# Kernel tuning notes

Hardware: AMD Instinct MI355X
Metric: run time of the kernel (lower is better)

The kernel has to match this reference:

```python
import jax, jax.numpy as jnp
import numpy as np
from jax import lax

B, T, D, NL, NH, FF, NC, SMAX, MAXS = 4, 160000, 768, 12, 12, 2048, 100, 64, 200
CONV_SPEC = [(512, 10, 5), (512, 3, 2), (512, 3, 2), (512, 3, 2), (512, 2, 2), (512, 2, 2), (768, 2, 2)]
TP = 499  # frames after conv stack for T=160000


def _ln(x, w, b, eps=1e-5):
    m = x.mean(-1, keepdims=True)
    v = ((x - m) ** 2).mean(-1, keepdims=True)
    return (x - m) * lax.rsqrt(v + eps) * w + b


def setup_inputs() -> dict:
    key = jax.random.key(0)
    ks = iter(jax.random.split(key, 64))
    d = {}
    d['x'] = jax.random.normal(next(ks), (B, 1, T), jnp.float32)
    d['seg_bounds'] = jnp.sort(jax.random.randint(next(ks), (B, SMAX + 1), 0, TP), axis=-1)
    d['n_segs'] = jax.random.randint(next(ks), (B,), SMAX // 2, SMAX + 1)
    in_c = 1
    for i, (oc, k, s) in enumerate(CONV_SPEC):
        d[f'conv_w{i}'] = jax.random.normal(next(ks), (oc, in_c, k), jnp.float32) * 0.02
        d[f'conv_b{i}'] = jnp.zeros((oc,), jnp.float32)
        in_c = oc
    d['attn_v'] = jax.random.normal(next(ks), (D,), jnp.float32)  # torch.randn init
    d['pos_emb'] = jax.random.normal(next(ks), (MAXS, D), jnp.float32) * 0.02
    d['in_w'] = jax.random.normal(next(ks), (NL, 3 * D, D), jnp.float32) * 0.02
    d['in_b'] = jnp.zeros((NL, 3 * D), jnp.float32)
    d['out_w'] = jax.random.normal(next(ks), (NL, D, D), jnp.float32) * 0.02
    d['out_b'] = jnp.zeros((NL, D), jnp.float32)
    d['ff1_w'] = jax.random.normal(next(ks), (NL, FF, D), jnp.float32) * 0.02
    d['ff1_b'] = jnp.zeros((NL, FF), jnp.float32)
    d['ff2_w'] = jax.random.normal(next(ks), (NL, D, FF), jnp.float32) * 0.02
    d['ff2_b'] = jnp.zeros((NL, D), jnp.float32)
    d['ln1_w'] = jnp.ones((NL, D), jnp.float32)
    d['ln1_b'] = jnp.zeros((NL, D), jnp.float32)
    d['ln2_w'] = jnp.ones((NL, D), jnp.float32)
    d['ln2_b'] = jnp.zeros((NL, D), jnp.float32)
    d['fln_w'] = jnp.ones((D,), jnp.float32)
    d['fln_b'] = jnp.zeros((D,), jnp.float32)
    d['proj_w'] = jax.random.normal(next(ks), (NC, D), jnp.float32) * 0.02
    d['proj_b'] = jnp.zeros((NC,), jnp.float32)
    return d


def reference(x, seg_bounds, n_segs,
              conv_w0, conv_b0, conv_w1, conv_b1, conv_w2, conv_b2, conv_w3, conv_b3,
              conv_w4, conv_b4, conv_w5, conv_b5, conv_w6, conv_b6,
              attn_v, pos_emb, in_w, in_b, out_w, out_b,
              ff1_w, ff1_b, ff2_w, ff2_b, ln1_w, ln1_b, ln2_w, ln2_b,
              fln_w, fln_b, proj_w, proj_b):
    # ---- conv feature extractor (Conv1d + ReLU stack), NCW layout ----
    ws = [conv_w0, conv_w1, conv_w2, conv_w3, conv_w4, conv_w5, conv_w6]
    bs = [conv_b0, conv_b1, conv_b2, conv_b3, conv_b4, conv_b5, conv_b6]
    h = x
    for w, b, (_, _, s) in zip(ws, bs, CONV_SPEC):
        h = lax.conv_general_dilated(h, w, (s,), 'VALID',
                                     dimension_numbers=('NCH', 'OIH', 'NCH'))
        h = jax.nn.relu(h + b[None, :, None])
    feats = h.transpose(0, 2, 1)  # [B, Tp, D]
    Tp = feats.shape[1]

    # ---- vectorized per-segment attention pooling (replaces ragged python loop) ----
    starts = jnp.clip(seg_bounds[:, :-1], 0, Tp - 1)           # [B, Smax]
    ends = jnp.maximum(starts + 1, jnp.clip(seg_bounds[:, 1:], 0, Tp))
    pad_mask = jnp.arange(SMAX)[None, :] >= n_segs[:, None]    # [B, Smax] True=pad
    t = jnp.arange(Tp)
    fm = (t[None, None, :] >= starts[..., None]) & (t[None, None, :] < ends[..., None]) \
         & (~pad_mask[..., None])                              # [B, Smax, Tp]
    scores = jnp.einsum('btc,c->bt', feats, attn_v)[:, None, :]  # [B, 1, Tp]
    m = jnp.max(jnp.where(fm, scores, -jnp.inf), axis=-1, keepdims=True)
    m = jnp.where(jnp.isfinite(m), m, 0.0)
    e = jnp.where(fm, jnp.exp(scores - m), 0.0)
    den = e.sum(-1, keepdims=True)
    wgt = e / jnp.where(den > 0, den, 1.0)                     # masked softmax over frames
    tokens = jnp.einsum('bst,btc->bsc', wgt, feats)            # [B, Smax, D]; pads are zeros

    tokens = tokens + pos_emb[:SMAX][None]

    # ---- post-norm transformer encoder (torch TransformerEncoderLayer defaults) ----
    dh = D // NH
    scale = 1.0 / np.sqrt(dh)

    def layer(tok, p):
        iw, ib, ow, ob, f1w, f1b, f2w, f2b, l1w, l1b, l2w, l2b = p
        qkv = tok @ iw.T + ib
        q, k, v = jnp.split(qkv, 3, axis=-1)
        def heads(z):
            return z.reshape(B, SMAX, NH, dh).transpose(0, 2, 1, 3)
        q, k, v = heads(q), heads(k), heads(v)
        att = jnp.einsum('bhqd,bhkd->bhqk', q, k) * scale
        att = jnp.where(pad_mask[:, None, None, :], -1e9, att)  # key padding mask
        att = jax.nn.softmax(att, axis=-1)
        o = jnp.einsum('bhqk,bhkd->bhqd', att, v).transpose(0, 2, 1, 3).reshape(B, SMAX, D)
        o = o @ ow.T + ob
        tok = _ln(tok + o, l1w, l1b)
        f = jax.nn.relu(tok @ f1w.T + f1b) @ f2w.T + f2b
        tok = _ln(tok + f, l2w, l2b)
        return tok, None

    tokens, _ = lax.scan(layer, tokens,
                         (in_w, in_b, out_w, out_b, ff1_w, ff1_b, ff2_w, ff2_b,
                          ln1_w, ln1_b, ln2_w, ln2_b))

    y = _ln(tokens, fln_w, fln_b)
    logits = y @ proj_w.T + proj_b
    return logits, pad_mask
```

## Files before the change

### kernel.cpp

```cpp
#include <hip/hip_runtime.h>
#include <hip/hip_bf16.h>

#define BATCH 4
#define TIN0 160000
#define DMODEL 768
#define NLAYER 12
#define FFDIM 2048
#define NCLS 100
#define SMAX_ 64
#define TP_ 499

typedef __attribute__((ext_vector_type(8))) short short8;
typedef __attribute__((ext_vector_type(4))) float f32x4;

__device__ inline ushort f2b(float f) { __hip_bfloat16 h = __float2bfloat16(f); return *(ushort*)&h; }
__device__ inline float b2f(ushort u) { __hip_bfloat16 h = *(__hip_bfloat16*)&u; return __bfloat162float(h); }

__device__ inline void gl_lds16(const ushort* g, ushort* l) {
    __builtin_amdgcn_global_load_lds((const __attribute__((address_space(1))) unsigned int*)g,
                                     (__attribute__((address_space(3))) unsigned int*)l, 16, 0, 0);
}

__device__ inline float wave_reduce_sum(float v) {
#pragma unroll
    for (int off = 32; off > 0; off >>= 1) v += __shfl_down(v, off, 64);
    return v;
}
__device__ inline float wave_reduce_max(float v) {
#pragma unroll
    for (int off = 32; off > 0; off >>= 1) v = fmaxf(v, __shfl_down(v, off, 64));
    return v;
}
__device__ inline float block_reduce_sum(float v, float* scratch) {
    v = wave_reduce_sum(v);
    int wid = threadIdx.x >> 6;
    if ((threadIdx.x & 63) == 0) scratch[wid] = v;
    __syncthreads();
    float r = scratch[0] + scratch[1] + scratch[2] + scratch[3];
    __syncthreads();
    return r;
}
__device__ inline float block_reduce_max(float v, float* scratch) {
    v = wave_reduce_max(v);
    int wid = threadIdx.x >> 6;
    if ((threadIdx.x & 63) == 0) scratch[wid] = v;
    __syncthreads();
    float r = fmaxf(fmaxf(scratch[0], scratch[1]), fmaxf(scratch[2], scratch[3]));
    __syncthreads();
    return r;
}

template <int KW>
__global__ __launch_bounds__(256) void convT_mfma(
    const ushort* __restrict__ A,
    const ushort* __restrict__ Wc,
    const float* __restrict__ bias,
    ushort* __restrict__ outp,
    int Cin, int Cout, int Tout,
    int tBase, int uBase, int uMax,
    long aStride, long oStride) {
    constexpr int EB = 132;
    __shared__ ushort sA[288 * 64];
    __shared__ ushort sB[KW * 128 * 32];
    const int tid = threadIdx.x;
    const int lane = tid & 63;
    const int wv = tid >> 6;
    const int mrow = lane & 15;
    const int kq = lane >> 4;
    const int t0 = tBase + blockIdx.x * 128;
    const int oc0 = blockIdx.y * 128;
    const ushort* Ab = A + (size_t)blockIdx.z * aStride;
    ushort* outb = outp + (size_t)blockIdx.z * oStride;
    const int K = KW * Cin;

    f32x4 acc[2][8];
#pragma unroll
    for (int s = 0; s < 2; s++)
#pragma unroll
        for (int n = 0; n < 8; n++) acc[s][n] = (f32x4){0.f, 0.f, 0.f, 0.f};

    const int nC8 = Cin >> 6;
    for (int c8 = 0; c8 < nC8; c8++) {
        const int ic0 = c8 << 6;
#pragma unroll
        for (int rd = 0; rd < 9; rd++) {
            int slotBase = rd * 256 + wv * 64;
            int slot = slotBase + lane;
            int r = slot >> 3;
            int g = (slot & 7) ^ (r & 7);
            int u = (r < EB) ? (2 * t0 + 2 * r) : (2 * t0 + 2 * (r - EB) + 1);
            u -= uBase;
            if (u < 0) u = 0;
            if (u > uMax) u = uMax;
            gl_lds16(Ab + (size_t)u * Cin + ic0 + g * 8, &sA[slotBase * 8]);
        }
#pragma unroll
        for (int h = 0; h < 2; h++) {
#pragma unroll
            for (int rd = 0; rd < KW * 2; rd++) {
                int slotBase = rd * 256 + wv * 64;
                int slot = slotBase + lane;
                int r = slot >> 2;
                int g = (slot & 3) ^ ((r >> 1) & 3);
                int ocr = oc0 + (r & 127);
                if (ocr > Cout - 1) ocr = Cout - 1;
                int kwi = r >> 7;
                gl_lds16(Wc + (size_t)ocr * K + kwi * Cin + ic0 + h * 32 + g * 8,
                         &sB[slotBase * 8]);
            }
            __syncthreads();
#pragma unroll
            for (int kw = 0; kw < KW; kw++) {
                const int abase = (kw & 1) ? EB : 0;
                const int aoff = kw >> 1;
#pragma unroll
                for (int s = 0; s < 2; s++) {
                    int ar = abase + wv * 32 + s * 16 + mrow + aoff;
                    short8 af = *(const short8*)&sA[ar * 64 + (((h * 4 + kq) ^ (ar & 7)) * 8)];
#pragma unroll
                    for (int n = 0; n < 8; n++) {
                        int br = kw * 128 + n * 16 + mrow;
                        short8 bf = *(const short8*)&sB[br * 32 + ((kq ^ ((br >> 1) & 3)) * 8)];
                        acc[s][n] = __builtin_amdgcn_mfma_f32_16x16x32_bf16(af, bf, acc[s][n], 0, 0, 0);
                    }
                }
            }
            __syncthreads();
        }
    }

    float bz[8];
#pragma unroll
    for (int n = 0; n < 8; n++) {
        int oc = oc0 + n * 16 + mrow;
        bz[n] = (oc < Cout) ? bias[oc] : 0.f;
    }
#pragma unroll
    for (int s = 0; s < 2; s++) {
        int tb = t0 + wv * 32 + s * 16 + kq * 4;
#pragma unroll
        for (int n = 0; n < 8; n++) {
            int oc = oc0 + n * 16 + mrow;
            if (oc >= Cout) continue;
#pragma unroll
            for (int r = 0; r < 4; r++) {
                int t = tb + r;
                if (t < Tout) outb[(size_t)t * Cout + oc] = f2b(fmaxf(acc[s][n][r] + bz[n], 0.f));
            }
        }
    }
}

template <int KW, int STRIDE, int RELU, int OBF, int BF32>
__global__ __launch_bounds__(256) void conv_mfma(
    const ushort* __restrict__ A,
    const ushort* __restrict__ Wc,
    const float* __restrict__ Wf,
    const float* __restrict__ bias,
    void* __restrict__ outv,
    int Cin, int Cout, int Tout, int tBase, int uBase,
    long aStride, long oStride) {
    const int K = KW * Cin;
    const int nCh = K >> 5;
    const int t0 = tBase + blockIdx.x * 128;
    const int oc0 = blockIdx.y * 128;
    const int b = blockIdx.z;
    const ushort* Ab = A + (size_t)b * aStride;
    __shared__ ushort sA[4096];
    __shared__ ushort sB[4096];
    const int tid = threadIdx.x;
    const int lane = tid & 63;
    const int wv = tid >> 6;
    const int rsub = lane >> 2;
    const int kgW = (lane & 3) ^ ((lane >> 3) & 3);
    const int mrow = lane & 15;
    const int kq = lane >> 4;
    const int slot8 = (mrow * 4 + (kq ^ ((mrow >> 1) & 3))) * 8;

    f32x4 acc[2][8];
#pragma unroll
    for (int s = 0; s < 2; s++)
#pragma unroll
        for (int n = 0; n < 8; n++) acc[s][n] = (f32x4){0.f, 0.f, 0.f, 0.f};

    for (int c = 0; c < nCh; c++) {
#pragma unroll
        for (int j = 0; j < 2; j++) {
            int t = t0 + j * 64 + wv * 16 + rsub;
            if (t > Tout - 1) t = Tout - 1;
            int u = STRIDE * t - uBase;
            gl_lds16(Ab + (size_t)u * Cin + c * 32 + kgW * 8, &sA[(j * 64 + wv * 16) * 32]);
        }
#pragma unroll
        for (int j = 0; j < 2; j++) {
            int rowb = oc0 + j * 64 + wv * 16 + rsub;
            if (rowb > Cout - 1) rowb = Cout - 1;
            if (BF32) {
                const float* wp = Wf + (size_t)rowb * K + c * 32 + kgW * 8;
                float4 w0_ = *(const float4*)wp;
                float4 w1_ = *(const float4*)(wp + 4);
                short8 vals;
                vals[0] = (short)f2b(w0_.x); vals[1] = (short)f2b(w0_.y);
                vals[2] = (short)f2b(w0_.z); vals[3] = (short)f2b(w0_.w);
                vals[4] = (short)f2b(w1_.x); vals[5] = (short)f2b(w1_.y);
                vals[6] = (short)f2b(w1_.z); vals[7] = (short)f2b(w1_.w);
                *(short8*)&sB[(j * 64 + wv * 16) * 32 + lane * 8] = vals;
            } else {
                gl_lds16(Wc + (size_t)rowb * K + c * 32 + kgW * 8, &sB[(j * 64 + wv * 16) * 32]);
            }
        }
        __syncthreads();
        short8 a0 = *(const short8*)&sA[(wv * 32 + 0) * 32 + slot8];
        short8 a1 = *(const short8*)&sA[(wv * 32 + 16) * 32 + slot8];
#pragma unroll
        for (int n = 0; n < 8; n++) {
            short8 bf = *(const short8*)&sB[(n * 16) * 32 + slot8];
            acc[0][n] = __builtin_amdgcn_mfma_f32_16x16x32_bf16(a0, bf, acc[0][n], 0, 0, 0);
            acc[1][n] = __builtin_amdgcn_mfma_f32_16x16x32_bf16(a1, bf, acc[1][n], 0, 0, 0);
        }
        __syncthreads();
    }
    float* outf = (float*)outv + (size_t)b * oStride;
    ushort* outh = (ushort*)outv + (size_t)b * oStride;
    float bz[8];
#pragma unroll
    for (int n = 0; n < 8; n++) {
        int oc = oc0 + n * 16 + mrow;
        bz[n] = (oc < Cout) ? bias[oc] : 0.f;
    }
#pragma unroll
    for (int s = 0; s < 2; s++) {
        int tb = t0 + wv * 32 + s * 16 + kq * 4;
#pragma unroll
        for (int n = 0; n < 8; n++) {
            int oc = oc0 + n * 16 + mrow;
            if (oc >= Cout) continue;
#pragma unroll
            for (int r = 0; r < 4; r++) {
                int t = tb + r;
                if (t < Tout) {
                    float v = acc[s][n][r] + bz[n];
                    if (RELU) v = fmaxf(v, 0.f);
                    if (OBF) outh[(size_t)t * Cout + oc] = f2b(v);
                    else outf[(size_t)t * Cout + oc] = v;
                }
            }
        }
    }
}

__global__ __launch_bounds__(256) void gemm_sk(
    const ushort* __restrict__ A, const float* __restrict__ Wf,
    const float* __restrict__ bias, float* __restrict__ outp,
    int M, int K, int KCH, long oSlab) {
    __shared__ ushort sA[4096];
    __shared__ ushort sB[4096];
    const int tid = threadIdx.x;
    const int lane = tid & 63;
    const int wv = tid >> 6;
    const int rsub = lane >> 2;
    const int kgW = (lane & 3) ^ ((lane >> 3) & 3);
    const int mrow = lane & 15;
    const int kq = lane >> 4;
    const int slot8 = (mrow * 4 + (kq ^ ((mrow >> 1) & 3))) * 8;
    const int t0 = blockIdx.x * 128;
    const int oc0 = blockIdx.y * 128;
    const int kc = blockIdx.z;
    const int k0 = kc * KCH;

    f32x4 acc[2][8];
#pragma unroll
    for (int s = 0; s < 2; s++)
#pragma unroll
        for (int n = 0; n < 8; n++) acc[s][n] = (f32x4){0.f, 0.f, 0.f, 0.f};

    const int nIt = KCH >> 5;
    for (int c = 0; c < nIt; c++) {
        const int kk = k0 + (c << 5);
#pragma unroll
        for (int j = 0; j < 2; j++) {
            int t = t0 + j * 64 + wv * 16 + rsub;
            gl_lds16(A + (size_t)t * K + kk + kgW * 8, &sA[(j * 64 + wv * 16) * 32]);
        }
#pragma unroll
        for (int j = 0; j < 2; j++) {
            int rowb = oc0 + j * 64 + wv * 16 + rsub;
            const float* wp = Wf + (size_t)rowb * K + kk + kgW * 8;
            float4 w0_ = *(const float4*)wp;
            float4 w1_ = *(const float4*)(wp + 4);
            short8 vals;
            vals[0] = (short)f2b(w0_.x); vals[1] = (short)f2b(w0_.y);
            vals[2] = (short)f2b(w0_.z); vals[3] = (short)f2b(w0_.w);
            vals[4] = (short)f2b(w1_.x); vals[5] = (short)f2b(w1_.y);
            vals[6] = (short)f2b(w1_.z); vals[7] = (short)f2b(w1_.w);
            *(short8*)&sB[(j * 64 + wv * 16) * 32 + lane * 8] = vals;
        }
        __syncthreads();
        short8 a0 = *(const short8*)&sA[(wv * 32 + 0) * 32 + slot8];
        short8 a1 = *(const short8*)&sA[(wv * 32 + 16) * 32 + slot8];
#pragma unroll
        for (int n = 0; n < 8; n++) {
            short8 bf = *(const short8*)&sB[(n * 16) * 32 + slot8];
            acc[0][n] = __builtin_amdgcn_mfma_f32_16x16x32_bf16(a0, bf, acc[0][n], 0, 0, 0);
            acc[1][n] = __builtin_amdgcn_mfma_f32_16x16x32_bf16(a1, bf, acc[1][n], 0, 0, 0);
        }
        __syncthreads();
    }

    float* op = outp + (size_t)kc * oSlab;
#pragma unroll
    for (int s = 0; s < 2; s++) {
        int tb = t0 + wv * 32 + s * 16 + kq * 4;
#pragma unroll
        for (int n = 0; n < 8; n++) {
            int oc = oc0 + n * 16 + mrow;
            float bz = (kc == 0) ? bias[oc] : 0.f;
#pragma unroll
            for (int r = 0; r < 4; r++) {
                op[(size_t)(tb + r) * M + oc] = acc[s][n][r] + bz;
            }
        }
    }
}

__global__ __launch_bounds__(256) void relu_cast(const float* __restrict__ p,
                                                 ushort* __restrict__ o,
                                                 long n, long slab, int nP) {
    for (long i = (long)blockIdx.x * 1024 + threadIdx.x; i < n; i += (long)gridDim.x * 1024) {
#pragma unroll
        for (int j = 0; j < 4; j++) {
            long k = i + (long)j * 256;
            if (k < n) {
                float v = 0.f;
                for (int q = 0; q < nP; q++) v += p[k + q * slab];
                o[k] = f2b(fmaxf(v, 0.f));
            }
        }
    }
}

__global__ __launch_bounds__(256) void conv0_mfma(const float* __restrict__ x,
                                                  const ushort* __restrict__ w0pad,
                                                  const float* __restrict__ b0,
                                                  ushort* __restrict__ c0,
                                                  int uBase, int nU) {
    __shared__ ushort sA[4096];
    __shared__ ushort sB[4096];
    const int tid = threadIdx.x;
    const int lane = tid & 63;
    const int wv = tid >> 6;
    const int rsub = lane >> 2;
    const int kgW = (lane & 3) ^ ((lane >> 3) & 3);
    const int mrow = lane & 15;
    const int kq = lane >> 4;
    const int slot8 = (mrow * 4 + (kq ^ ((mrow >> 1) & 3))) * 8;
    const int r0 = blockIdx.x * 128;
    const int oc0 = blockIdx.y * 128;

    f32x4 acc[2][8];
#pragma unroll
    for (int s = 0; s < 2; s++)
#pragma unroll
        for (int n = 0; n < 8; n++) acc[s][n] = (f32x4){0.f, 0.f, 0.f, 0.f};

#pragma unroll
    for (int j = 0; j < 2; j++) {
        int r = r0 + j * 64 + wv * 16 + rsub;
        if (r > nU - 1) r = nU - 1;
        const float* xp = x + (size_t)5 * (uBase + r);
        short8 vals = (short8){0, 0, 0, 0, 0, 0, 0, 0};
        if (kgW == 0) {
#pragma unroll
            for (int q = 0; q < 8; q++) vals[q] = (short)f2b(xp[q]);
        } else if (kgW == 1) {
            vals[0] = (short)f2b(xp[8]);
            vals[1] = (short)f2b(xp[9]);
        }
        *(short8*)&sA[(j * 64 + wv * 16) * 32 + lane * 8] = vals;
    }
#pragma unroll
    for (int j = 0; j < 2; j++) {
        int rowb = oc0 + j * 64 + wv * 16 + rsub;
        gl_lds16(w0pad + (size_t)rowb * 32 + kgW * 8, &sB[(j * 64 + wv * 16) * 32]);
    }
    __syncthreads();
    short8 a0 = *(const short8*)&sA[(wv * 32 + 0) * 32 + slot8];
    short8 a1 = *(const short8*)&sA[(wv * 32 + 16) * 32 + slot8];
#pragma unroll
    for (int n = 0; n < 8; n++) {
        short8 bf = *(const short8*)&sB[(n * 16) * 32 + slot8];
        acc[0][n] = __builtin_amdgcn_mfma_f32_16x16x32_bf16(a0, bf, acc[0][n], 0, 0, 0);
        acc[1][n] = __builtin_amdgcn_mfma_f32_16x16x32_bf16(a1, bf, acc[1][n], 0, 0, 0);
    }
#pragma unroll
    for (int s = 0; s < 2; s++) {
        int rb = r0 + wv * 32 + s * 16 + kq * 4;
#pragma unroll
        for (int n = 0; n < 8; n++) {
            int oc = oc0 + n * 16 + mrow;
            float bz = b0[oc];
#pragma unroll
            for (int r = 0; r < 4; r++) {
                int rr = rb + r;
                if (rr < nU) c0[(size_t)rr * 512 + oc] = f2b(fmaxf(acc[s][n][r] + bz, 0.f));
            }
        }
    }
}

__global__ __launch_bounds__(256) void convw_kernel(
    const float* __restrict__ w1, const float* __restrict__ w2, const float* __restrict__ w3,
    const float* __restrict__ w4, const float* __restrict__ w5, const float* __restrict__ w6,
    const float* __restrict__ w0, ushort* __restrict__ dst, ushort* __restrict__ dw0) {
    const int z = blockIdx.y;
    const int COUTS[6] = {512, 512, 512, 512, 512, 768};
    const int KWS[6] = {3, 3, 3, 2, 2, 2};
    const long OFFS[6] = {0, 786432, 1572864, 2359296, 2883584, 3407872};
    const float* srcs[6] = {w1, w2, w3, w4, w5, w6};
    if (z == 6) {
        for (int o = blockIdx.x * 256 + threadIdx.x; o < 512 * 32; o += gridDim.x * 256) {
            int oc = o >> 5, q = o & 31;
            dw0[o] = (q < 10) ? f2b(w0[oc * 10 + q]) : (ushort)0;
        }
        return;
    }
    const float* src = srcs[z];
    ushort* d = dst + OFFS[z];
    const int Cin = 512, Kw = KWS[z];
    const int K = Cin * Kw;
    const long n = (long)COUTS[z] * K;
    for (long o = blockIdx.x * 256 + threadIdx.x; o < n; o += (long)gridDim.x * 256) {
        long oc = o / K;
        int rem = (int)(o - oc * K);
        int kw = rem / Cin, ic = rem - kw * Cin;
        d[o] = f2b(src[(oc * Cin + ic) * Kw + kw]);
    }
}

__global__ __launch_bounds__(256) void scores_kernel(const ushort* __restrict__ feats,
                                                     const float* __restrict__ v,
                                                     float* __restrict__ scores) {
    int b = blockIdx.y;
    int t = blockIdx.x * 4 + (threadIdx.x >> 6);
    if (t >= TP_) return;
    int lane = threadIdx.x & 63;
    const ushort* f = feats + ((size_t)b * TP_ + t) * DMODEL + lane * 12;
    float acc = 0.f;
#pragma unroll
    for (int q = 0; q < 12; q++) acc = fmaf(b2f(f[q]), v[lane * 12 + q], acc);
    acc = wave_reduce_sum(acc);
    if (lane == 0) scores[b * TP_ + t] = acc;
}

__global__ __launch_bounds__(256) void pool_kernel(const ushort* __restrict__ featsAll,
                                                   const float* __restrict__ scoresAll,
                                                   const int* __restrict__ seg_bounds,
                                                   const int* __restrict__ n_segs,
                                                   const float* __restrict__ pos_emb,
                                                   float* __restrict__ tokens,
                                                   ushort* __restrict__ tokens_bf) {
    __shared__ float scratch[4];
    __shared__ float wgt[512];
    int s = blockIdx.x, b = blockIdx.y, tid = threadIdx.x;
    float* tout = tokens + ((size_t)b * SMAX_ + s) * DMODEL;
    ushort* tbf = tokens_bf + ((size_t)b * SMAX_ + s) * DMODEL;
    int ns = n_segs[b];
    if (s >= ns) {
        for (int c = tid; c < DMODEL; c += 256) {
            float v = pos_emb[s * DMODEL + c];
            tout[c] = v; tbf[c] = f2b(v);
        }
        return;
    }
    const float* sc = scoresAll + b * TP_;
    int b0 = seg_bounds[b * (SMAX_ + 1) + s];
    int b1 = seg_bounds[b * (SMAX_ + 1) + s + 1];
    int st = min(max(b0, 0), TP_ - 1);
    int en = max(st + 1, min(max(b1, 0), TP_));
    float lm = -1e30f;
    for (int t = st + tid; t < en; t += 256) lm = fmaxf(lm, sc[t]);
    float m = block_reduce_max(lm, scratch);
    float ls = 0.f;
    for (int t = st + tid; t < en; t += 256) ls += __expf(sc[t] - m);
    float den = block_reduce_sum(ls, scratch);
    float inv = 1.f / den;
    for (int t = st + tid; t < en; t += 256) wgt[t - st] = __expf(sc[t] - m) * inv;
    __syncthreads();
    int len = en - st;
    const ushort* f = featsAll + ((size_t)b * TP_ + st) * DMODEL;
    float a0 = 0.f, a1 = 0.f, a2 = 0.f;
    for (int t = 0; t < len; t++) {
        float wv = wgt[t];
        const ushort* fr = f + (size_t)t * DMODEL;
        a0 = fmaf(wv, b2f(fr[tid]), a0);
        a1 = fmaf(wv, b2f(fr[tid + 256]), a1);
        a2 = fmaf(wv, b2f(fr[tid + 512]), a2);
    }
    float v0 = a0 + pos_emb[s * DMODEL + tid];
    float v1 = a1 + pos_emb[s * DMODEL + tid + 256];
    float v2 = a2 + pos_emb[s * DMODEL + tid + 512];
    tout[tid] = v0; tout[tid + 256] = v1; tout[tid + 512] = v2;
    tbf[tid] = f2b(v0); tbf[tid + 256] = f2b(v1); tbf[tid + 512] = f2b(v2);
}

__global__ __launch_bounds__(256) void attn_kernel(const float* __restrict__ qkv_p,
                                                   const int* __restrict__ n_segs,
                                                   ushort* __restrict__ o, long slab, int nP) {
    __shared__ float sK[64][68];
    __shared__ float sV[64][68];
    __shared__ float sS[64][68];
    int h = blockIdx.x, b = blockIdx.y, tid = threadIdx.x;
    int ns = n_segs[b];
    const float* base = qkv_p + (size_t)b * 64 * 2304 + h * 64;
    for (int idx = tid; idx < 4096; idx += 256) {
        int s_ = idx >> 6, d = idx & 63;
        size_t kofs = (size_t)s_ * 2304 + 768 + d;
        size_t vofs = (size_t)s_ * 2304 + 1536 + d;
        float kv = 0.f, vv = 0.f;
        for (int p = 0; p < nP; p++) { kv += base[kofs + p * slab]; vv += base[vofs + p * slab]; }
        sK[s_][d] = kv; sV[s_][d] = vv;
    }
    __syncthreads();
    int qr = tid >> 2;
    int c0 = (tid & 3) * 16;
    const float* qrow = base + (size_t)qr * 2304;
    float acc[16];
#pragma unroll
    for (int j = 0; j < 16; j++) acc[j] = 0.f;
    for (int d = 0; d < 64; d += 4) {
        float4 qv = make_float4(0.f, 0.f, 0.f, 0.f);
        for (int p = 0; p < nP; p++) {
            float4 qp = *(const float4*)(qrow + p * slab + d);
            qv.x += qp.x; qv.y += qp.y; qv.z += qp.z; qv.w += qp.w;
        }
#pragma unroll
        for (int j = 0; j < 16; j++) {
            float4 kv = *(const float4*)&sK[c0 + j][d];
            acc[j] += qv.x * kv.x + qv.y * kv.y + qv.z * kv.z + qv.w * kv.w;
        }
    }
#pragma unroll
    for (int j = 0; j < 16; j++) {
        int kc = c0 + j;
        float vv = acc[j] * 0.125f;
        if (kc >= ns) vv = -1e9f;
        sS[qr][kc] = vv;
    }
    __syncthreads();
    if (tid < 64) {
        float m = -1e30f;
#pragma unroll 4
        for (int k = 0; k < 64; k++) m = fmaxf(m, sS[tid][k]);
        float ssum = 0.f;
#pragma unroll 4
        for (int k = 0; k < 64; k++) {
            float e = __expf(sS[tid][k] - m);
            sS[tid][k] = e;
            ssum += e;
        }
        float inv = 1.f / ssum;
#pragma unroll 4
        for (int k = 0; k < 64; k++) sS[tid][k] *= inv;
    }
    __syncthreads();
    float4 oacc[4];
#pragma unroll
    for (int j = 0; j < 4; j++) oacc[j] = make_float4(0.f, 0.f, 0.f, 0.f);
    for (int k = 0; k < 64; k++) {
        float wv = sS[qr][k];
#pragma unroll
        for (int j4 = 0; j4 < 4; j4++) {
            float4 vv = *(const float4*)&sV[k][c0 + j4 * 4];
            oacc[j4].x = fmaf(wv, vv.x, oacc[j4].x);
            oacc[j4].y = fmaf(wv, vv.y, oacc[j4].y);
            oacc[j4].z = fmaf(wv, vv.z, oacc[j4].z);
            oacc[j4].w = fmaf(wv, vv.w, oacc[j4].w);
        }
    }
    ushort* orow = o + ((size_t)b * 64 + qr) * DMODEL + h * 64 + c0;
#pragma unroll
    for (int j4 = 0; j4 < 4; j4++) {
        orow[j4 * 4 + 0] = f2b(oacc[j4].x);
        orow[j4 * 4 + 1] = f2b(oacc[j4].y);
        orow[j4 * 4 + 2] = f2b(oacc[j4].z);
        orow[j4 * 4 + 3] = f2b(oacc[j4].w);
    }
}

__global__ __launch_bounds__(256) void ln_kernel(const float* __restrict__ x,
                                                 const float* __restrict__ rP, int nP, long rSlab,
                                                 const float* __restrict__ w,
                                                 const float* __restrict__ b,
                                                 float* __restrict__ out,
                                                 ushort* __restrict__ outbf) {
    __shared__ float scratch[4];
    int row = blockIdx.x, tid = threadIdx.x;
    const float* xr = x + (size_t)row * DMODEL;
    float v0 = xr[tid], v1 = xr[tid + 256], v2 = xr[tid + 512];
    for (int p = 0; p < nP; p++) {
        const float* rr = rP + (size_t)p * rSlab + (size_t)row * DMODEL;
        v0 += rr[tid]; v1 += rr[tid + 256]; v2 += rr[tid + 512];
    }
    float mean = block_reduce_sum(v0 + v1 + v2, scratch) * (1.f / DMODEL);
    float d0 = v0 - mean, d1 = v1 - mean, d2 = v2 - mean;
    float var = block_reduce_sum(d0 * d0 + d1 * d1 + d2 * d2, scratch) * (1.f / DMODEL);
    float inv = rsqrtf(var + 1e-5f);
    float o0 = d0 * inv * w[tid] + b[tid];
    float o1 = d1 * inv * w[tid + 256] + b[tid + 256];
    float o2 = d2 * inv * w[tid + 512] + b[tid + 512];
    float* orow = out + (size_t)row * DMODEL;
    orow[tid] = o0; orow[tid + 256] = o1; orow[tid + 512] = o2;
    if (outbf) {
        ushort* obf = outbf + (size_t)row * DMODEL;
        obf[tid] = f2b(o0); obf[tid + 256] = f2b(o1); obf[tid + 512] = f2b(o2);
    }
}

__global__ void mask_kernel(const int* __restrict__ n_segs, float* __restrict__ mout) {
    int i = threadIdx.x;
    int b = i >> 6, s = i & 63;
    mout[i] = (s >= n_segs[b]) ? 1.0f : 0.0f;
}

extern "C" void kernel_launch(void* const* d_in, const int* in_sizes, int n_in,
                              void* d_out, int out_size, void* d_ws, size_t ws_size,
                              hipStream_t stream) {
    const float* x = (const float*)d_in[0];
    const int* seg_bounds = (const int*)d_in[1];
    const int* n_segs = (const int*)d_in[2];
    const float* cw[7], * cb[7];
    for (int i = 0; i < 7; i++) { cw[i] = (const float*)d_in[3 + 2 * i]; cb[i] = (const float*)d_in[4 + 2 * i]; }
    const float* attn_v = (const float*)d_in[17];
    const float* pos_emb = (const float*)d_in[18];
    const float* in_w = (const float*)d_in[19];
    const float* in_b = (const float*)d_in[20];
    const float* out_w = (const float*)d_in[21];
    const float* out_b = (const float*)d_in[22];
    const float* ff1_w = (const float*)d_in[23];
    const float* ff1_b = (const float*)d_in[24];
    const float* ff2_w = (const float*)d_in[25];
    const float* ff2_b = (const float*)d_in[26];
    const float* ln1_w = (const float*)d_in[27];
    const float* ln1_b = (const float*)d_in[28];
    const float* ln2_w = (const float*)d_in[29];
    const float* ln2_b = (const float*)d_in[30];
    const float* fln_w = (const float*)d_in[31];
    const float* fln_b = (const float*)d_in[32];
    const float* proj_w = (const float*)d_in[33];
    const float* proj_b = (const float*)d_in[34];

    mask_kernel<<<1, 256, 0, stream>>>(n_segs, (float*)d_out + 256 * NCLS);

    size_t off = 0;
    auto alloc = [&](size_t bytes) {
        void* p = (char*)d_ws + off;
        off += (bytes + 255) & ~(size_t)255;
        return p;
    };
    ushort* wbc = (ushort*)alloc(4194304ULL * 2);
    ushort* w0pad = (ushort*)alloc(512ULL * 32 * 2);
    ushort* c0buf = (ushort*)alloc((size_t)16001 * 512 * 2);
    ushort* out1 = (ushort*)alloc((size_t)15999 * 512 * 2);
    ushort* out4 = (ushort*)alloc((size_t)4 * 1999 * 512 * 2);
    float* scores = (float*)alloc((size_t)4 * TP_ * 4);
    float* tokens = (float*)alloc((size_t)256 * DMODEL * 4);
    ushort* tokens_bf = (ushort*)alloc((size_t)256 * DMODEL * 2);
    ushort* oall_bf = (ushort*)alloc((size_t)256 * DMODEL * 2);
    float* ybuf = (float*)alloc((size_t)256 * DMODEL * 4);
    ushort* ybf = (ushort*)alloc((size_t)256 * DMODEL * 2);
    if (off > ws_size) return;

    ushort* out2b = c0buf;
    ushort* out3b = out1 + (size_t)12000 * 512;
    ushort* out5 = c0buf;
    ushort* feats = out1;
    float* qkv_p = (float*)c0buf;
    float* ffh_p = (float*)c0buf + (size_t)4 * 256 * 2304;
    ushort* ffh_bf = (ushort*)out4;
    float* tmp_p = (float*)((char*)out4 + (size_t)256 * 2048 * 2);

    ushort* wc1 = wbc, * wc2 = wbc + 786432, * wc3 = wbc + 1572864,
          * wc4 = wbc + 2359296, * wc5 = wbc + 2883584, * wc6 = wbc + 3407872;

    convw_kernel<<<dim3(512, 7), 256, 0, stream>>>(cw[1], cw[2], cw[3], cw[4], cw[5], cw[6],
                                                   cw[0], wbc, w0pad);

    for (int b = 0; b < BATCH; b++) {
        const float* xb = x + (size_t)b * TIN0;
        conv0_mfma<<<dim3(126, 4), 256, 0, stream>>>(xb, w0pad, cb[0], c0buf, 0, 16001);
        convT_mfma<3><<<dim3(63, 4, 1), 256, 0, stream>>>(
            c0buf, wc1, cb[1], out1, 512, 512, 15999, 0, 0, 16000, 0, 0);
        conv0_mfma<<<dim3(125, 4), 256, 0, stream>>>(xb, w0pad, cb[0], c0buf, 16000, 15999);
        convT_mfma<3><<<dim3(63, 4, 1), 256, 0, stream>>>(
            c0buf, wc1, cb[1], out1, 512, 512, 15999, 8000, 16000, 15998, 0, 0);
        convT_mfma<3><<<dim3(63, 4, 1), 256, 0, stream>>>(
            out1, wc2, cb[2], out2b, 512, 512, 7999, 0, 0, 15998, 0, 0);
        convT_mfma<3><<<dim3(32, 4, 1), 256, 0, stream>>>(
            out2b, wc3, cb[3], out3b, 512, 512, 3999, 0, 0, 7998, 0, 0);
        convT_mfma<2><<<dim3(16, 4, 1), 256, 0, stream>>>(
            out3b, wc4, cb[4], out4 + (size_t)b * 1999 * 512, 512, 512, 1999, 0, 0, 3998, 0, 0);
    }
    convT_mfma<2><<<dim3(8, 4, BATCH), 256, 0, stream>>>(
        out4, wc5, cb[5], out5, 512, 512, 999, 0, 0, 1998,
        (long)1999 * 512, (long)999 * 512);
    convT_mfma<2><<<dim3(4, 6, BATCH), 256, 0, stream>>>(
        out5, wc6, cb[6], feats, 512, 768, 499, 0, 0, 998,
        (long)999 * 512, (long)499 * 768);

    scores_kernel<<<dim3(125, 4), 256, 0, stream>>>(feats, attn_v, scores);
    pool_kernel<<<dim3(SMAX_, 4), 256, 0, stream>>>(feats, scores, seg_bounds, n_segs,
                                                    pos_emb, tokens, tokens_bf);

    const long qkvSlab = (long)256 * 2304;
    const long tmpSlab = (long)256 * 768;
    const long ffhSlab = (long)256 * 2048;
    for (int l = 0; l < NLAYER; l++) {
        const float* iw = in_w + (size_t)l * 2304 * DMODEL;
        const float* ib = in_b + (size_t)l * 2304;
        const float* ow = out_w + (size_t)l * DMODEL * DMODEL;
        const float* ob = out_b + (size_t)l * DMODEL;
        const float* f1w = ff1_w + (size_t)l * FFDIM * DMODEL;
        const float* f1b = ff1_b + (size_t)l * FFDIM;
        const float* f2w = ff2_w + (size_t)l * DMODEL * FFDIM;
        const float* f2b_ = ff2_b + (size_t)l * DMODEL;

        gemm_sk<<<dim3(2, 18, 4), 256, 0, stream>>>(tokens_bf, iw, ib, qkv_p, 2304, 768, 192, qkvSlab);
        attn_kernel<<<dim3(12, 4), 256, 0, stream>>>(qkv_p, n_segs, oall_bf, qkvSlab, 4);
        gemm_sk<<<dim3(2, 6, 4), 256, 0, stream>>>(oall_bf, ow, ob, tmp_p, 768, 768, 192, tmpSlab);
        ln_kernel<<<256, 256, 0, stream>>>(tokens, tmp_p, 4, tmpSlab,
                                           ln1_w + l * DMODEL, ln1_b + l * DMODEL, tokens, tokens_bf);
        gemm_sk<<<dim3(2, 16, 3), 256, 0, stream>>>(tokens_bf, f1w, f1b, ffh_p, 2048, 768, 256, ffhSlab);
        relu_cast<<<512, 256, 0, stream>>>(ffh_p, ffh_bf, (long)256 * 2048, ffhSlab, 3);
        gemm_sk<<<dim3(2, 6, 8), 256, 0, stream>>>(ffh_bf, f2w, f2b_, tmp_p, 768, 2048, 256, tmpSlab);
        ln_kernel<<<256, 256, 0, stream>>>(tokens, tmp_p, 8, tmpSlab,
                                           ln2_w + l * DMODEL, ln2_b + l * DMODEL, tokens, tokens_bf);
    }

    ln_kernel<<<256, 256, 0, stream>>>(tokens, nullptr, 0, 0, fln_w, fln_b, ybuf, ybf);
    conv_mfma<1, 1, 0, 0, 1><<<dim3(2, 1, 1), 256, 0, stream>>>(
        ybf, nullptr, proj_w, proj_b, (float*)d_out, 768, NCLS, 256, 0, 0, 0, 0);
}
```

Measured before the change: 2.560 ms.

## Batch conv stack across batch via grid z and double-buffer transformer GEMM

The conv front-end now launches each conv stage once with the batch on grid z, instead of looping over the four batch items. This needs separate per-stage buffers for all batches rather than reused scratch. The transformer split-K GEMM is replaced by a version where each block covers all 256 token rows, which halves the block count and reads each weight tile once instead of twice. That GEMM also double-buffers LDS and prefetches the next A tile and weight registers while MFMAs run. The trade-off is fewer blocks per GEMM, more LDS and more accumulator registers per thread, and a larger workspace footprint.

```diff
diff --git a/kernel.cpp b/kernel.cpp
--- a/kernel.cpp
+++ b/kernel.cpp
@@ -249,12 +249,12 @@
     }
 }
 
-__global__ __launch_bounds__(256) void gemm_sk(
+__global__ __launch_bounds__(256) void gemm_sk2(
     const ushort* __restrict__ A, const float* __restrict__ Wf,
     const float* __restrict__ bias, float* __restrict__ outp,
     int M, int K, int KCH, long oSlab) {
-    __shared__ ushort sA[4096];
-    __shared__ ushort sB[4096];
+    __shared__ ushort sA[2][8192];
+    __shared__ ushort sB[2][4096];
     const int tid = threadIdx.x;
     const int lane = tid & 63;
     const int wv = tid >> 6;
@@ -263,54 +263,79 @@
     const int mrow = lane & 15;
     const int kq = lane >> 4;
     const int slot8 = (mrow * 4 + (kq ^ ((mrow >> 1) & 3))) * 8;
-    const int t0 = blockIdx.x * 128;
     const int oc0 = blockIdx.y * 128;
     const int kc = blockIdx.z;
     const int k0 = kc * KCH;
-
-    f32x4 acc[2][8];
-#pragma unroll
-    for (int s = 0; s < 2; s++)
+    const int nIt = KCH >> 5;
+
+    f32x4 acc[4][8];
+#pragma unroll
+    for (int s = 0; s < 4; s++)
 #pragma unroll
         for (int n = 0; n < 8; n++) acc[s][n] = (f32x4){0.f, 0.f, 0.f, 0.f};
 
-    const int nIt = KCH >> 5;
-    for (int c = 0; c < nIt; c++) {
-        const int kk = k0 + (c << 5);
-#pragma unroll
-        for (int j = 0; j < 2; j++) {
-            int t = t0 + j * 64 + wv * 16 + rsub;
-            gl_lds16(A + (size_t)t * K + kk + kgW * 8, &sA[(j * 64 + wv * 16) * 32]);
-        }
+    float4 wr[2][2];
+
+    auto stageA = [&](int buf, int kk) {
+#pragma unroll
+        for (int j = 0; j < 4; j++) {
+            int t = j * 64 + wv * 16 + rsub;
+            gl_lds16(A + (size_t)t * K + kk + kgW * 8, &sA[buf][(j * 64 + wv * 16) * 32]);
+        }
+    };
+    auto wload = [&](int kk) {
 #pragma unroll
         for (int j = 0; j < 2; j++) {
             int rowb = oc0 + j * 64 + wv * 16 + rsub;
             const float* wp = Wf + (size_t)rowb * K + kk + kgW * 8;
-            float4 w0_ = *(const float4*)wp;
-            float4 w1_ = *(const float4*)(wp + 4);
+            wr[j][0] = *(const float4*)wp;
+            wr[j][1] = *(const float4*)(wp + 4);
+        }
+    };
+    auto wstore = [&](int buf) {
+#pragma unroll
+        for (int j = 0; j < 2; j++) {
             short8 vals;
-            vals[0] = (short)f2b(w0_.x); vals[1] = (short)f2b(w0_.y);
-            vals[2] = (short)f2b(w0_.z); vals[3] = (short)f2b(w0_.w);
-            vals[4] = (short)f2b(w1_.x); vals[5] = (short)f2b(w1_.y);
-            vals[6] = (short)f2b(w1_.z); vals[7] = (short)f2b(w1_.w);
-            *(short8*)&sB[(j * 64 + wv * 16) * 32 + lane * 8] = vals;
-        }
-        __syncthreads();
-        short8 a0 = *(const short8*)&sA[(wv * 32 + 0) * 32 + slot8];
-        short8 a1 = *(const short8*)&sA[(wv * 32 + 16) * 32 + slot8];
+            vals[0] = (short)f2b(wr[j][0].x); vals[1] = (short)f2b(wr[j][0].y);
+            vals[2] = (short)f2b(wr[j][0].z); vals[3] = (short)f2b(wr[j][0].w);
+            vals[4] = (short)f2b(wr[j][1].x); vals[5] = (short)f2b(wr[j][1].y);
+            vals[6] = (short)f2b(wr[j][1].z); vals[7] = (short)f2b(wr[j][1].w);
+            *(short8*)&sB[buf][(j * 64 + wv * 16) * 32 + lane * 8] = vals;
+        }
+    };
+
+    stageA(0, k0);
+    wload(k0);
+    wstore(0);
+    __syncthreads();
+
+    for (int c = 0; c < nIt; c++) {
+        const int cur = c & 1;
+        const int nxt = cur ^ 1;
+        if (c + 1 < nIt) {
+            stageA(nxt, k0 + ((c + 1) << 5));
+            wload(k0 + ((c + 1) << 5));
+        }
+        short8 a0 = *(const short8*)&sA[cur][(wv * 64 + 0) * 32 + slot8];
+        short8 a1 = *(const short8*)&sA[cur][(wv * 64 + 16) * 32 + slot8];
+        short8 a2 = *(const short8*)&sA[cur][(wv * 64 + 32) * 32 + slot8];
+        short8 a3 = *(const short8*)&sA[cur][(wv * 64 + 48) * 32 + slot8];
 #pragma unroll
         for (int n = 0; n < 8; n++) {
-            short8 bf = *(const short8*)&sB[(n * 16) * 32 + slot8];
+            short8 bf = *(const short8*)&sB[cur][(n * 16) * 32 + slot8];
             acc[0][n] = __builtin_amdgcn_mfma_f32_16x16x32_bf16(a0, bf, acc[0][n], 0, 0, 0);
             acc[1][n] = __builtin_amdgcn_mfma_f32_16x16x32_bf16(a1, bf, acc[1][n], 0, 0, 0);
-        }
+            acc[2][n] = __builtin_amdgcn_mfma_f32_16x16x32_bf16(a2, bf, acc[2][n], 0, 0, 0);
+            acc[3][n] = __builtin_amdgcn_mfma_f32_16x16x32_bf16(a3, bf, acc[3][n], 0, 0, 0);
+        }
+        if (c + 1 < nIt) wstore(nxt);
         __syncthreads();
     }
 
     float* op = outp + (size_t)kc * oSlab;
 #pragma unroll
-    for (int s = 0; s < 2; s++) {
-        int tb = t0 + wv * 32 + s * 16 + kq * 4;
+    for (int s = 0; s < 4; s++) {
+        int tb = wv * 64 + s * 16 + kq * 4;
 #pragma unroll
         for (int n = 0; n < 8; n++) {
             int oc = oc0 + n * 16 + mrow;
@@ -343,7 +368,7 @@
                                                   const ushort* __restrict__ w0pad,
                                                   const float* __restrict__ b0,
                                                   ushort* __restrict__ c0,
-                                                  int uBase, int nU) {
+                                                  int uBase, int nU, long oStride) {
     __shared__ ushort sA[4096];
     __shared__ ushort sB[4096];
     const int tid = threadIdx.x;
@@ -356,6 +381,8 @@
     const int slot8 = (mrow * 4 + (kq ^ ((mrow >> 1) & 3))) * 8;
     const int r0 = blockIdx.x * 128;
     const int oc0 = blockIdx.y * 128;
+    const float* xb = x + (size_t)blockIdx.z * TIN0;
+    ushort* ob = c0 + (size_t)blockIdx.z * oStride;
 
     f32x4 acc[2][8];
 #pragma unroll
@@ -367,7 +394,7 @@
     for (int j = 0; j < 2; j++) {
         int r = r0 + j * 64 + wv * 16 + rsub;
         if (r > nU - 1) r = nU - 1;
-        const float* xp = x + (size_t)5 * (uBase + r);
+        const float* xp = xb + (size_t)5 * (uBase + r);
         short8 vals = (short8){0, 0, 0, 0, 0, 0, 0, 0};
         if (kgW == 0) {
 #pragma unroll
@@ -402,7 +429,7 @@
 #pragma unroll
             for (int r = 0; r < 4; r++) {
                 int rr = rb + r;
-                if (rr < nU) c0[(size_t)rr * 512 + oc] = f2b(fmaxf(acc[s][n][r] + bz, 0.f));
+                if (rr < nU) ob[(size_t)rr * 512 + oc] = f2b(fmaxf(acc[s][n][r] + bz, 0.f));
             }
         }
     }
@@ -657,11 +684,17 @@
         off += (bytes + 255) & ~(size_t)255;
         return p;
     };
+    const long c0S = 16001L * 512, o1S = 16000L * 512, o2S = 8000L * 512,
+               o3S = 4000L * 512, o4S = 2000L * 512, o5S = 1000L * 512, fS = 499L * 768;
     ushort* wbc = (ushort*)alloc(4194304ULL * 2);
     ushort* w0pad = (ushort*)alloc(512ULL * 32 * 2);
-    ushort* c0buf = (ushort*)alloc((size_t)16001 * 512 * 2);
-    ushort* out1 = (ushort*)alloc((size_t)15999 * 512 * 2);
-    ushort* out4 = (ushort*)alloc((size_t)4 * 1999 * 512 * 2);
+    ushort* c0_all = (ushort*)alloc((size_t)BATCH * c0S * 2);
+    ushort* o1 = (ushort*)alloc((size_t)BATCH * o1S * 2);
+    ushort* o2 = (ushort*)alloc((size_t)BATCH * o2S * 2);
+    ushort* o3 = (ushort*)alloc((size_t)BATCH * o3S * 2);
+    ushort* o4 = (ushort*)alloc((size_t)BATCH * o4S * 2);
+    ushort* o5 = (ushort*)alloc((size_t)BATCH * o5S * 2);
+    ushort* feats = (ushort*)alloc((size_t)BATCH * fS * 2);
     float* scores = (float*)alloc((size_t)4 * TP_ * 4);
     float* tokens = (float*)alloc((size_t)256 * DMODEL * 4);
     ushort* tokens_bf = (ushort*)alloc((size_t)256 * DMODEL * 2);
@@ -670,14 +703,10 @@
     ushort* ybf = (ushort*)alloc((size_t)256 * DMODEL * 2);
     if (off > ws_size) return;
 
-    ushort* out2b = c0buf;
-    ushort* out3b = out1 + (size_t)12000 * 512;
-    ushort* out5 = c0buf;
-    ushort* feats = out1;
-    float* qkv_p = (float*)c0buf;
-    float* ffh_p = (float*)c0buf + (size_t)4 * 256 * 2304;
-    ushort* ffh_bf = (ushort*)out4;
-    float* tmp_p = (float*)((char*)out4 + (size_t)256 * 2048 * 2);
+    float* qkv_p = (float*)c0_all;
+    float* ffh_p = qkv_p + (size_t)4 * 256 * 2304;
+    float* tmp_p = ffh_p + (size_t)3 * 256 * 2048;
+    ushort* ffh_bf = (ushort*)(tmp_p + (size_t)8 * 256 * 768);
 
     ushort* wc1 = wbc, * wc2 = wbc + 786432, * wc3 = wbc + 1572864,
           * wc4 = wbc + 2359296, * wc5 = wbc + 2883584, * wc6 = wbc + 3407872;
@@ -685,27 +714,22 @@
     convw_kernel<<<dim3(512, 7), 256, 0, stream>>>(cw[1], cw[2], cw[3], cw[4], cw[5], cw[6],
                                                    cw[0], wbc, w0pad);
 
-    for (int b = 0; b < BATCH; b++) {
-        const float* xb = x + (size_t)b * TIN0;
-        conv0_mfma<<<dim3(126, 4), 256, 0, stream>>>(xb, w0pad, cb[0], c0buf, 0, 16001);
-        convT_mfma<3><<<dim3(63, 4, 1), 256, 0, stream>>>(
-            c0buf, wc1, cb[1], out1, 512, 512, 15999, 0, 0, 16000, 0, 0);
-        conv0_mfma<<<dim3(125, 4), 256, 0, stream>>>(xb, w0pad, cb[0], c0buf, 16000, 15999);
-        convT_mfma<3><<<dim3(63, 4, 1), 256, 0, stream>>>(
-            c0buf, wc1, cb[1], out1, 512, 512, 15999, 8000, 16000, 15998, 0, 0);
-        convT_mfma<3><<<dim3(63, 4, 1), 256, 0, stream>>>(
-            out1, wc2, cb[2], out2b, 512, 512, 7999, 0, 0, 15998, 0, 0);
-        convT_mfma<3><<<dim3(32, 4, 1), 256, 0, stream>>>(
-            out2b, wc3, cb[3], out3b, 512, 512, 3999, 0, 0, 7998, 0, 0);
-        convT_mfma<2><<<dim3(16, 4, 1), 256, 0, stream>>>(
-            out3b, wc4, cb[4], out4 + (size_t)b * 1999 * 512, 512, 512, 1999, 0, 0, 3998, 0, 0);
-    }
+    conv0_mfma<<<dim3(126, 4, BATCH), 256, 0, stream>>>(x, w0pad, cb[0], c0_all, 0, 16001, c0S);
+    convT_mfma<3><<<dim3(63, 4, BATCH), 256, 0, stream>>>(
+        c0_all, wc1, cb[1], o1, 512, 512, 15999, 0, 0, 16000, c0S, o1S);
+    conv0_mfma<<<dim3(125, 4, BATCH), 256, 0, stream>>>(x, w0pad, cb[0], c0_all, 16000, 15999, c0S);
+    convT_mfma<3><<<dim3(63, 4, BATCH), 256, 0, stream>>>(
+        c0_all, wc1, cb[1], o1, 512, 512, 15999, 8000, 16000, 15998, c0S, o1S);
+    convT_mfma<3><<<dim3(63, 4, BATCH), 256, 0, stream>>>(
+        o1, wc2, cb[2], o2, 512, 512, 7999, 0, 0, 15998, o1S, o2S);
+    convT_mfma<3><<<dim3(32, 4, BATCH), 256, 0, stream>>>(
+        o2, wc3, cb[3], o3, 512, 512, 3999, 0, 0, 7998, o2S, o3S);
+    convT_mfma<2><<<dim3(16, 4, BATCH), 256, 0, stream>>>(
+        o3, wc4, cb[4], o4, 512, 512, 1999, 0, 0, 3998, o3S, o4S);
     convT_mfma<2><<<dim3(8, 4, BATCH), 256, 0, stream>>>(
-        out4, wc5, cb[5], out5, 512, 512, 999, 0, 0, 1998,
-        (long)1999 * 512, (long)999 * 512);
+        o4, wc5, cb[5], o5, 512, 512, 999, 0, 0, 1998, o4S, o5S);
     convT_mfma<2><<<dim3(4, 6, BATCH), 256, 0, stream>>>(
-        out5, wc6, cb[6], feats, 512, 768, 499, 0, 0, 998,
-        (long)999 * 512, (long)499 * 768);
+        o5, wc6, cb[6], feats, 512, 768, 499, 0, 0, 998, o5S, fS);
 
     scores_kernel<<<dim3(125, 4), 256, 0, stream>>>(feats, attn_v, scores);
     pool_kernel<<<dim3(SMAX_, 4), 256, 0, stream>>>(feats, scores, seg_bounds, n_segs,
@@ -724,14 +748,14 @@
         const float* f2w = ff2_w + (size_t)l * DMODEL * FFDIM;
         const float* f2b_ = ff2_b + (size_t)l * DMODEL;
 
-        gemm_sk<<<dim3(2, 18, 4), 256, 0, stream>>>(tokens_bf, iw, ib, qkv_p, 2304, 768, 192, qkvSlab);
+        gemm_sk2<<<dim3(1, 18, 4), 256, 0, stream>>>(tokens_bf, iw, ib, qkv_p, 2304, 768, 192, qkvSlab);
         attn_kernel<<<dim3(12, 4), 256, 0, stream>>>(qkv_p, n_segs, oall_bf, qkvSlab, 4);
-        gemm_sk<<<dim3(2, 6, 4), 256, 0, stream>>>(oall_bf, ow, ob, tmp_p, 768, 768, 192, tmpSlab);
+        gemm_sk2<<<dim3(1, 6, 4), 256, 0, stream>>>(oall_bf, ow, ob, tmp_p, 768, 768, 192, tmpSlab);
         ln_kernel<<<256, 256, 0, stream>>>(tokens, tmp_p, 4, tmpSlab,
                                            ln1_w + l * DMODEL, ln1_b + l * DMODEL, tokens, tokens_bf);
-        gemm_sk<<<dim3(2, 16, 3), 256, 0, stream>>>(tokens_bf, f1w, f1b, ffh_p, 2048, 768, 256, ffhSlab);
+        gemm_sk2<<<dim3(1, 16, 3), 256, 0, stream>>>(tokens_bf, f1w, f1b, ffh_p, 2048, 768, 256, ffhSlab);
         relu_cast<<<512, 256, 0, stream>>>(ffh_p, ffh_bf, (long)256 * 2048, ffhSlab, 3);
-        gemm_sk<<<dim3(2, 6, 8), 256, 0, stream>>>(ffh_bf, f2w, f2b_, tmp_p, 768, 2048, 256, tmpSlab);
+        gemm_sk2<<<dim3(1, 6, 8), 256, 0, stream>>>(ffh_bf, f2w, f2b_, tmp_p, 768, 2048, 256, tmpSlab);
         ln_kernel<<<256, 256, 0, stream>>>(tokens, tmp_p, 8, tmpSlab,
                                            ln2_w + l * DMODEL, ln2_b + l * DMODEL, tokens, tokens_bf);
     }
```

Result: faster. 2.339 ms (-8.6%).
